# Optimization experiments

Hardware: AMD Instinct MI355X
Metric: run time of the kernel (lower is better)

The kernel has to match this reference:

```python
import jax, jax.numpy as jnp
import numpy as np

N, E = 30000, 240000          # nodes, edges per view
IN, D, OUT = 512, 128, 64      # in_dim, hidden_dim, out_dim
V, BLK, H, DM = 2, 2, 2, 64    # num_view, blk_size, num_heads, gate max-pool dim
NEG_ATT, NEG_OUT = 0.2, 0.01   # leaky_relu slopes (attention / outer)


def setup_inputs() -> dict:
    key = jax.random.key(0)
    ks = jax.random.split(key, 12)
    s = 0.05
    f32 = jnp.float32
    return {
        "ft": jax.random.normal(ks[0], (N, IN), f32),
        "src": jax.random.randint(ks[1], (V, E), 0, N, jnp.int32),
        "dst": jax.random.randint(ks[2], (V, E), 0, N, jnp.int32),
        "W_proj": jax.random.normal(ks[3], (IN, D), f32) * s,
        "W_embed": jax.random.normal(ks[4], (D, D), f32) * s,
        "a_l": jax.random.normal(ks[5], (V, BLK, H, D), f32) * s,
        "a_r": jax.random.normal(ks[6], (V, BLK, H, D), f32) * s,
        "Wv": jax.random.normal(ks[7], (V, BLK, H, D, D), f32) * s,
        "Wgm": jax.random.normal(ks[8], (V, BLK, D, DM), f32) * s,
        "Wgate": jax.random.normal(ks[9], (V, BLK, 2 * D + DM, H), f32) * s,
        "b_gate": jnp.zeros((V, BLK, H), f32),
        "W_tran": jax.random.normal(ks[10], (2 * D + DM and (D + V * H * D), OUT), f32) * s if False else jax.random.normal(ks[10], (D + V * H * D, OUT), f32) * s,
        "b_tran": jnp.zeros((OUT,), f32),
    }


def _seg_sum(x, idx):
    return jax.ops.segment_sum(x, idx, num_segments=N)


def _cgaan_layer(v, z, s_idx, d_idx, al, ar, wv, wgm, wgate, bg, merge):
    # v: [N,D] values, z: [N,D] attention features ('proj_z')
    # Multi-head attention logits: e_ij = leaky_relu(a_l.z_src + a_r.z_dst)  [E,H]
    logit_l = jnp.einsum("nd,hd->nh", z, al)
    logit_r = jnp.einsum("nd,hd->nh", z, ar)
    e = jax.nn.leaky_relu(logit_l[s_idx] + logit_r[d_idx], NEG_ATT)
    # edge softmax over incoming edges of each dst node
    m = jax.ops.segment_max(e, d_idx, num_segments=N)          # [N,H]
    ex = jnp.exp(e - m[d_idx])
    denom = _seg_sum(ex, d_idx)                                 # [N,H]
    alpha = ex / denom[d_idx]                                   # [E,H]
    # per-head value projection and weighted aggregation
    wvn = jnp.einsum("nd,hde->nhe", v, wv)                      # [N,H,D]
    agg = _seg_sum(alpha[:, :, None] * wvn[s_idx], d_idx)       # [N,H,D]
    # GaAN-style gate: sigmoid(FC([x_i, mean_j v_j, max_j (v_j Wgm)])) -> per-head scalar
    deg = _seg_sum(jnp.ones((s_idx.shape[0],), v.dtype), d_idx)  # [N]
    mean_n = _seg_sum(v[s_idx], d_idx) / jnp.maximum(deg, 1.0)[:, None]
    mx = jax.ops.segment_max((v @ wgm)[s_idx], d_idx, num_segments=N)
    mx = jnp.where(deg[:, None] > 0, mx, 0.0)                   # isolated nodes -> 0
    g = jax.nn.sigmoid(jnp.concatenate([v, mean_n, mx], -1) @ wgate + bg)  # [N,H]
    agg = g[:, :, None] * agg
    if merge == "mean":
        return agg.mean(axis=1)                                 # [N,D]
    return agg.reshape(agg.shape[0], -1)                        # cat -> [N,H*D]


def reference(ft, src, dst, W_proj, W_embed, a_l, a_r, Wv, Wgm, Wgate, b_gate, W_tran, b_tran):
    proj = ft @ W_proj                                          # [N,D]
    cur = [proj for _ in range(V)]
    for i in range(BLK):
        merge = "mean" if i < BLK - 1 else "cat"
        nxt = []
        for j in range(V):
            z = cur[j] @ W_embed
            h = _cgaan_layer(cur[j], z, src[j], dst[j], a_l[j, i], a_r[j, i],
                             Wv[j, i], Wgm[j, i], Wgate[j, i], b_gate[j, i], merge)
            nxt.append(jax.nn.leaky_relu(h, NEG_OUT))
        cur = nxt
    h = jnp.concatenate([proj] + cur, axis=-1)                  # [N, D+V*H*D]
    return h @ W_tran + b_tran
```

## Files before the change

### kernel.cpp

```cpp
#include <hip/hip_runtime.h>
#include <hip/hip_bf16.h>
#include <math.h>

#define NN 30000
#define EE 240000
#define IN_DIM 512
#define DD 128
#define OUTD 64
#define NV 2
#define NBLK 2
#define NH 2
#define DMM 64
#define NEG_ATT 0.2f
#define NEG_OUT 0.01f
#define CH 1024
#define NCH ((NN + CH - 1) / CH)

typedef __attribute__((ext_vector_type(8))) short bf16x8;
typedef __attribute__((ext_vector_type(4))) float f32x4;
typedef __attribute__((ext_vector_type(8))) unsigned short us8;

#define OFF_PROJVM 0
#define OFF_WV     131072
#define OFF_WGM    262144
#define OFF_TRAN   278528
#define WT_TOTAL   319488

__device__ __forceinline__ unsigned split_bf(float x) {
  unsigned u = __float_as_uint(x);
  unsigned hb = (u + 0x7FFFu + ((u >> 16) & 1u)) >> 16;
  float hf = __uint_as_float(hb << 16);
  float lo = x - hf;
  unsigned ul = __float_as_uint(lo);
  unsigned lb = (ul + 0x7FFFu + ((ul >> 16) & 1u)) >> 16;
  return hb | (lb << 16);
}

__device__ __forceinline__ void gload16(void* lds, const void* g) {
  __builtin_amdgcn_global_load_lds((const __attribute__((address_space(1))) unsigned int*)g,
                                   (__attribute__((address_space(3))) unsigned int*)lds, 16, 0, 0);
}

__global__ __launch_bounds__(256) void k_deg(const int* __restrict__ dst, int* __restrict__ deg) {
  int e = blockIdx.x * 256 + threadIdx.x;
  if (e < NV * EE) atomicAdd(&deg[(e / EE) * NN + dst[e]], 1);
}

__global__ __launch_bounds__(256) void k_scan1(const int* __restrict__ deg, int* __restrict__ partial) {
  int b = blockIdx.x, view = b / NCH, ch = b % NCH;
  const int* d = deg + view * NN + ch * CH;
  int rem = min(CH, NN - ch * CH);
  int t = threadIdx.x;
  int s = 0;
  for (int i = t; i < rem; i += 256) s += d[i];
  for (int k = 32; k; k >>= 1) s += __shfl_xor(s, k);
  __shared__ int wsum[4];
  if ((t & 63) == 0) wsum[t >> 6] = s;
  __syncthreads();
  if (t == 0) partial[b] = wsum[0] + wsum[1] + wsum[2] + wsum[3];
}

__global__ void k_scan2(const int* __restrict__ partial, int* __restrict__ chunkoff, int* __restrict__ off) {
  if (threadIdx.x == 0 && blockIdx.x == 0) {
    for (int v = 0; v < NV; v++) {
      int acc = 0;
      for (int c = 0; c < NCH; c++) { chunkoff[v * NCH + c] = acc; acc += partial[v * NCH + c]; }
      off[v * (NN + 1) + NN] = acc;
    }
  }
}

__global__ __launch_bounds__(256) void k_scan3(const int* __restrict__ deg, const int* __restrict__ chunkoff,
                                               int* __restrict__ off) {
  int b = blockIdx.x, view = b / NCH, ch = b % NCH;
  int base = ch * CH;
  const int* d = deg + view * NN;
  int* o = off + view * (NN + 1);
  int t = threadIdx.x, lane = t & 63, w = t >> 6;
  int i0 = base + t * 4;
  int x0 = 0, x1 = 0, x2 = 0, x3 = 0;
  if (i0 + 3 < NN) { int4 q = *(const int4*)(d + i0); x0 = q.x; x1 = q.y; x2 = q.z; x3 = q.w; }
  else {
    if (i0     < NN) x0 = d[i0];
    if (i0 + 1 < NN) x1 = d[i0 + 1];
    if (i0 + 2 < NN) x2 = d[i0 + 2];
  }
  int tot = x0 + x1 + x2 + x3;
  int incl = tot;
  for (int k = 1; k < 64; k <<= 1) { int y = __shfl_up(incl, k); if (lane >= k) incl += y; }
  __shared__ int wt[4];
  if (lane == 63) wt[w] = incl;
  __syncthreads();
  int wexcl = 0;
  for (int k = 0; k < w; k++) wexcl += wt[k];
  int excl = chunkoff[b] + wexcl + incl - tot;
  if (i0     < NN) o[i0]     = excl;
  if (i0 + 1 < NN) o[i0 + 1] = excl + x0;
  if (i0 + 2 < NN) o[i0 + 2] = excl + x0 + x1;
  if (i0 + 3 < NN) o[i0 + 3] = excl + x0 + x1 + x2;
}

__global__ __launch_bounds__(256) void k_fill(const int* __restrict__ src, const int* __restrict__ dst,
                                              const int* __restrict__ off, int* __restrict__ cursor,
                                              int* __restrict__ csr_src) {
  int e = blockIdx.x * 256 + threadIdx.x;
  if (e >= NV * EE) return;
  int view = e / EE;
  int d = dst[e];
  int p = atomicAdd(&cursor[view * NN + d], 1);
  csr_src[view * EE + off[view * (NN + 1) + d] + p] = src[e];
}

__global__ __launch_bounds__(256) void k_prep(const float* __restrict__ W_embed, const float* __restrict__ a_l,
                                              const float* __restrict__ a_r, float* __restrict__ Bl,
                                              float* __restrict__ Br) {
  int idx = blockIdx.x * 256 + threadIdx.x;
  if (idx >= NV * NBLK * DD * NH) return;
  int h = idx & 1, dd = (idx >> 1) & 127, lv = idx >> 8;
  const float* w = W_embed + dd * DD;
  const float* al = a_l + (lv * NH + h) * DD;
  const float* ar = a_r + (lv * NH + h) * DD;
  float sl = 0.f, sr = 0.f;
  for (int e = 0; e < DD; e++) { float we = w[e]; sl += we * al[e]; sr += we * ar[e]; }
  Bl[idx] = sl; Br[idx] = sr;
}

__global__ __launch_bounds__(256) void k_prep2(const float* __restrict__ Wp, const float* __restrict__ Wgm,
                                               float* __restrict__ wf) {
  int idx = blockIdx.x * 256 + threadIdx.x;
  int j = idx >> 15, k = (idx >> 6) & 511, n = idx & 63;
  const float* wp = Wp + (size_t)k * DD;
  const float* wg = Wgm + (size_t)(j * NBLK + 0) * DD * DMM + n;
  float s = 0.f;
  for (int e = 0; e < DD; e++) s += wp[e] * wg[(size_t)e * DMM];
  wf[idx] = s;
}

__global__ __launch_bounds__(256) void k_wsplit(const float* __restrict__ Wp, const float* __restrict__ wf,
                                                const float* __restrict__ Wv, const float* __restrict__ Wgm,
                                                const float* __restrict__ Wt,
                                                unsigned short* __restrict__ hi, unsigned short* __restrict__ lo) {
  int y = blockIdx.y;
  const float* src; int K, N; size_t doff;
  if (y == 0)      { src = Wp;                      K = 512; N = 128; doff = OFF_PROJVM; }
  else if (y <= 2) { int j = y - 1; src = wf + (size_t)j * 512 * 64; K = 512; N = 64; doff = OFF_PROJVM + (size_t)(128 + j * 64) * 512; }
  else if (y <= 6) { int lv = y - 3; src = Wv + (size_t)lv * 32768;  K = 256; N = 128; doff = OFF_WV + (size_t)lv * 32768; }
  else if (y <= 8) { int j = y - 7; src = Wgm + (size_t)(j * NBLK + 1) * 8192; K = 128; N = 64; doff = OFF_WGM + (size_t)j * 8192; }
  else             { src = Wt;                      K = 640; N = 64;  doff = OFF_TRAN; }
  int idx = blockIdx.x * 256 + threadIdx.x;
  if (idx >= K * N) return;
  int n = idx / K, k = idx % K;
  int tk = k >> 6, g = (k >> 3) & 7, j2 = k & 7;
  int ks = (tk << 6) | ((g ^ (n & 7)) << 3) | j2;
  unsigned p = split_bf(src[(size_t)k * N + n]);
  hi[doff + (size_t)n * K + ks] = (unsigned short)(p & 0xFFFFu);
  lo[doff + (size_t)n * K + ks] = (unsigned short)(p >> 16);
}

__global__ __launch_bounds__(256) void k_llr(const float* __restrict__ v0, const float* __restrict__ v1,
                                             int vstride,
                                             const float* __restrict__ Bl0, const float* __restrict__ Br0,
                                             const float* __restrict__ Bl1, const float* __restrict__ Br1,
                                             float* __restrict__ ll, float* __restrict__ lr) {
  int lane = threadIdx.x & 63, wid = threadIdx.x >> 6;
  int n = blockIdx.x * 4 + wid;
  int k = lane * 2;
  float2 a = *(const float2*)(v0 + (size_t)n * vstride + k);
  float2 b = *(const float2*)(v1 + (size_t)n * vstride + k);
  float r[8];
  r[0] = a.x * Bl0[k * 2]     + a.y * Bl0[k * 2 + 2];
  r[1] = a.x * Bl0[k * 2 + 1] + a.y * Bl0[k * 2 + 3];
  r[2] = a.x * Br0[k * 2]     + a.y * Br0[k * 2 + 2];
  r[3] = a.x * Br0[k * 2 + 1] + a.y * Br0[k * 2 + 3];
  r[4] = b.x * Bl1[k * 2]     + b.y * Bl1[k * 2 + 2];
  r[5] = b.x * Bl1[k * 2 + 1] + b.y * Bl1[k * 2 + 3];
  r[6] = b.x * Br1[k * 2]     + b.y * Br1[k * 2 + 2];
  r[7] = b.x * Br1[k * 2 + 1] + b.y * Br1[k * 2 + 3];
  for (int s = 32; s; s >>= 1)
#pragma unroll
    for (int q = 0; q < 8; q++) r[q] += __shfl_xor(r[q], s);
  if (lane == 0) {
    ll[n * 2] = r[0]; ll[n * 2 + 1] = r[1];
    lr[n * 2] = r[2]; lr[n * 2 + 1] = r[3];
    ll[NN * 2 + n * 2] = r[4]; ll[NN * 2 + n * 2 + 1] = r[5];
    lr[NN * 2 + n * 2] = r[6]; lr[NN * 2 + n * 2 + 1] = r[7];
  }
}

__global__ __launch_bounds__(256) void k_edge(const int* __restrict__ off_, const int* __restrict__ csr_,
                                              const float* __restrict__ ll_, const float* __restrict__ lr_,
                                              const float* __restrict__ v0, const float* __restrict__ v1,
                                              int vstride,
                                              const float* __restrict__ vmin,
                                              const float* __restrict__ Wg_, const float* __restrict__ bg_,
                                              float* __restrict__ S_) {
  int view = blockIdx.y;
  const int* off = off_ + view * (NN + 1);
  const int* csr = csr_ + (size_t)view * EE;
  const float* ll = ll_ + (size_t)view * NN * 2;
  const float* lr = lr_ + (size_t)view * NN * 2;
  const float* v = view ? v1 : v0;
  const float* vmi = vmin + view * 64;
  const float* Wg = Wg_ + (size_t)view * NBLK * (2 * DD + DMM) * NH;
  const float* bg = bg_ + view * NBLK * NH;
  float* S = S_ + (size_t)view * NN * (NH * DD);

  int lane = threadIdx.x & 63, wid = threadIdx.x >> 6;
  int n = blockIdx.x * 4 + wid;
  int e0 = off[n], nb = off[n + 1] - e0;
  size_t nS = (size_t)n * (NH * DD);
  int half = lane >> 5, hl = lane & 31;
  if (nb == 0) {
    *(float4*)(S + nS + half * DD + 4 * hl) = make_float4(0.f, 0.f, 0.f, 0.f);
    return;
  }
  float lr0 = lr[n * 2], lr1 = lr[n * 2 + 1];
  float sa0[4] = {0.f, 0.f, 0.f, 0.f}, sa1[4] = {0.f, 0.f, 0.f, 0.f}, vs[4] = {0.f, 0.f, 0.f, 0.f};
  float d0 = 0.f, d1 = 0.f, vm0 = -INFINITY, vm1 = -INFINITY;
  for (int base = 0; base < nb; base += 64) {
    int i = base + lane;
    float w0 = 0.f, w1 = 0.f, fv = 0.f; int sidx = 0;
    if (i < nb) {
      sidx = csr[e0 + i];
      float x0 = ll[sidx * 2] + lr0, x1 = ll[sidx * 2 + 1] + lr1;
      x0 = (x0 > 0.f) ? x0 : NEG_ATT * x0;
      x1 = (x1 > 0.f) ? x1 : NEG_ATT * x1;
      w0 = __expf(x0); w1 = __expf(x1); fv = 1.f;
    }
    d0 += w0; d1 += w1;
    int cnt = min(64, nb - base);
    for (int s = 0; 2 * s < cnt; s++) {
      int j = 2 * s + half;
      int se = __shfl(sidx, j);
      float we0 = __shfl(w0, j), we1 = __shfl(w1, j), fe = __shfl(fv, j);
      if (fe != 0.f) {
        float4 vv = *(const float4*)(v + (size_t)se * vstride + 4 * hl);
        sa0[0] += we0 * vv.x; sa0[1] += we0 * vv.y; sa0[2] += we0 * vv.z; sa0[3] += we0 * vv.w;
        sa1[0] += we1 * vv.x; sa1[1] += we1 * vv.y; sa1[2] += we1 * vv.z; sa1[3] += we1 * vv.w;
        vs[0] += vv.x; vs[1] += vv.y; vs[2] += vv.z; vs[3] += vv.w;
        float2 vm = *(const float2*)(vmi + (size_t)se * DD + 2 * hl);
        vm0 = fmaxf(vm0, vm.x); vm1 = fmaxf(vm1, vm.y);
      }
    }
  }
#pragma unroll
  for (int k = 0; k < 4; k++) {
    sa0[k] += __shfl_xor(sa0[k], 32);
    sa1[k] += __shfl_xor(sa1[k], 32);
    vs[k]  += __shfl_xor(vs[k], 32);
  }
  vm0 = fmaxf(vm0, __shfl_xor(vm0, 32));
  vm1 = fmaxf(vm1, __shfl_xor(vm1, 32));
  for (int s = 32; s; s >>= 1) { d0 += __shfl_xor(d0, s); d1 += __shfl_xor(d1, s); }
  float2 vn = *(const float2*)(v + (size_t)n * vstride + 2 * lane);
  float im = 1.f / (float)nb;
  float p0 = vn.x * Wg[(2 * lane) * 2]     + vn.y * Wg[(2 * lane + 1) * 2];
  float p1 = vn.x * Wg[(2 * lane) * 2 + 1] + vn.y * Wg[(2 * lane + 1) * 2 + 1];
  if (half == 0) {
#pragma unroll
    for (int k = 0; k < 4; k++) {
      float mk = vs[k] * im;
      p0 += mk * Wg[(128 + 4 * hl + k) * 2];
      p1 += mk * Wg[(128 + 4 * hl + k) * 2 + 1];
    }
  } else {
    p0 += vm0 * Wg[(256 + 2 * hl) * 2]     + vm1 * Wg[(256 + 2 * hl + 1) * 2];
    p1 += vm0 * Wg[(256 + 2 * hl) * 2 + 1] + vm1 * Wg[(256 + 2 * hl + 1) * 2 + 1];
  }
  for (int s = 32; s; s >>= 1) { p0 += __shfl_xor(p0, s); p1 += __shfl_xor(p1, s); }
  float g0 = 1.f / (1.f + __expf(-(p0 + bg[0])));
  float g1 = 1.f / (1.f + __expf(-(p1 + bg[1])));
  float q0 = g0 / d0, q1 = g1 / d1;
  float4 o4;
  if (half == 0) o4 = make_float4(sa0[0] * q0, sa0[1] * q0, sa0[2] * q0, sa0[3] * q0);
  else           o4 = make_float4(sa1[0] * q1, sa1[1] * q1, sa1[2] * q1, sa1[3] * q1);
  *(float4*)(S + nS + half * DD + 4 * hl) = o4;
}

struct GB {
  const float* A[4];
  unsigned long long bofs[4];
  float* C[4];
  int ldc[4];
};

template <int BN>
__global__ __launch_bounds__(256) void gemm_mfma(
    GB gb, const unsigned short* __restrict__ Bth, const unsigned short* __restrict__ Btl,
    int lda, int ldb, int M, int K,
    const float* __restrict__ bias, float fs, int flags) {
  constexpr int NSUB = BN / 32;
  constexpr int CPW = BN / 32;
  __shared__ __align__(16) unsigned short Ah[64][64], Al[64][64];
  __shared__ __align__(16) unsigned short Bh[BN][64], Bl[BN][64];
  const int z = blockIdx.z;
  const float* __restrict__ A = gb.A[z];
  float* __restrict__ C = gb.C[z];
  const int ldc = gb.ldc[z];
  const size_t bofs = gb.bofs[z];
  const int t = threadIdx.x;
  const int lane = t & 63, wv = t >> 6;
  const int lm = lane & 15, lg = lane >> 4;
  const int m0w = (wv & 1) * 32, n0w = (wv >> 1) * (BN / 2);
  const int row0 = blockIdx.x * 64;
  f32x4 acc[2][NSUB];
#pragma unroll
  for (int ms = 0; ms < 2; ms++)
#pragma unroll
    for (int ns = 0; ns < NSUB; ns++) acc[ms][ns] = (f32x4)0.f;

  float4 apre[2][2];
  const int ar_ = t >> 3, ag_ = t & 7;

  auto loadA = [&](int k0) {
#pragma unroll
    for (int q = 0; q < 2; q++) {
      int rr = row0 + q * 32 + ar_;
      if (rr < M) {
        const float* p = A + (size_t)rr * lda + k0 + ag_ * 8;
        apre[q][0] = *(const float4*)p;
        apre[q][1] = *(const float4*)(p + 4);
      } else {
        apre[q][0] = make_float4(0.f, 0.f, 0.f, 0.f);
        apre[q][1] = make_float4(0.f, 0.f, 0.f, 0.f);
      }
    }
  };
  auto storeA = [&]() {
#pragma unroll
    for (int q = 0; q < 2; q++) {
      int r = q * 32 + ar_;
      us8 h8, l8;
      float vals[8] = {apre[q][0].x, apre[q][0].y, apre[q][0].z, apre[q][0].w,
                       apre[q][1].x, apre[q][1].y, apre[q][1].z, apre[q][1].w};
#pragma unroll
      for (int e = 0; e < 8; e++) {
        unsigned pp = split_bf(vals[e]);
        h8[e] = (unsigned short)(pp & 0xFFFFu);
        l8[e] = (unsigned short)(pp >> 16);
      }
      int c = (ag_ ^ (r & 7)) << 3;
      *(us8*)&Ah[r][c] = h8;
      *(us8*)&Al[r][c] = l8;
    }
  };
  auto stageB = [&](int k0) {
#pragma unroll
    for (int q = 0; q < CPW; q++) {
      int chunk = wv * CPW + q;
      int o = chunk * 1024 + lane * 16;
      int n = o >> 7;
      int pq = (o >> 4) & 7;
      size_t gofs = bofs + (size_t)n * ldb + k0 + pq * 8;
      gload16((char*)&Bh[0][0] + o, Bth + gofs);
      gload16((char*)&Bl[0][0] + o, Btl + gofs);
    }
  };

  loadA(0);
  for (int k0 = 0; k0 < K; k0 += 64) {
    storeA();
    stageB(k0);
    __syncthreads();
    if (k0 + 64 < K) loadA(k0 + 64);
#pragma unroll
    for (int kc = 0; kc < 2; kc++) {
      bf16x8 afh[2], afl[2], bfh[NSUB], bfl[NSUB];
#pragma unroll
      for (int ms = 0; ms < 2; ms++) {
        int R = m0w + ms * 16 + lm;
        int c = (((kc * 4 + lg) ^ (R & 7)) << 3);
        afh[ms] = *(const bf16x8*)&Ah[R][c];
        afl[ms] = *(const bf16x8*)&Al[R][c];
      }
#pragma unroll
      for (int ns = 0; ns < NSUB; ns++) {
        int R = n0w + ns * 16 + lm;
        int c = (((kc * 4 + lg) ^ (R & 7)) << 3);
        bfh[ns] = *(const bf16x8*)&Bh[R][c];
        bfl[ns] = *(const bf16x8*)&Bl[R][c];
      }
#pragma unroll
      for (int ms = 0; ms < 2; ms++)
#pragma unroll
        for (int ns = 0; ns < NSUB; ns++) {
          acc[ms][ns] = __builtin_amdgcn_mfma_f32_16x16x32_bf16(afl[ms], bfh[ns], acc[ms][ns], 0, 0, 0);
          acc[ms][ns] = __builtin_amdgcn_mfma_f32_16x16x32_bf16(afh[ms], bfl[ns], acc[ms][ns], 0, 0, 0);
          acc[ms][ns] = __builtin_amdgcn_mfma_f32_16x16x32_bf16(afh[ms], bfh[ns], acc[ms][ns], 0, 0, 0);
        }
    }
    __syncthreads();
  }
#pragma unroll
  for (int ms = 0; ms < 2; ms++)
#pragma unroll
    for (int ns = 0; ns < NSUB; ns++)
#pragma unroll
      for (int j = 0; j < 4; j++) {
        int row = row0 + m0w + ms * 16 + lg * 4 + j;
        if (row >= M) continue;
        int col = n0w + ns * 16 + lm;
        float val = acc[ms][ns][j] * fs;
        if (bias) val += bias[col];
        if (flags & 2) val = (val > 0.f) ? val : NEG_OUT * val;
        C[(size_t)row * ldc + col] = val;
      }
}

extern "C" void kernel_launch(void* const* d_in, const int* in_sizes, int n_in,
                              void* d_out, int out_size, void* d_ws, size_t ws_size,
                              hipStream_t stream) {
  const float* ft      = (const float*)d_in[0];
  const int*   src     = (const int*)  d_in[1];
  const int*   dst     = (const int*)  d_in[2];
  const float* W_proj  = (const float*)d_in[3];
  const float* W_embed = (const float*)d_in[4];
  const float* a_l     = (const float*)d_in[5];
  const float* a_r     = (const float*)d_in[6];
  const float* Wv      = (const float*)d_in[7];
  const float* Wgm     = (const float*)d_in[8];
  const float* Wgate   = (const float*)d_in[9];
  const float* b_gate  = (const float*)d_in[10];
  const float* W_tran  = (const float*)d_in[11];
  const float* b_tran  = (const float*)d_in[12];
  float* out = (float*)d_out;
  char* ws = (char*)d_ws;
  (void)in_sizes; (void)n_in; (void)out_size; (void)ws_size;

  size_t o = 0;
  auto take = [&](size_t bytes) { size_t r = o; o += (bytes + 255) & ~(size_t)255; return r; };
  int*   deg     = (int*)(ws + take((size_t)NV * NN * 4));
  int*   cursor  = (int*)(ws + take((size_t)NV * NN * 4));
  int*   csr_off = (int*)(ws + take((size_t)NV * (NN + 1) * 4));
  int*   csr_src = (int*)(ws + take((size_t)NV * EE * 4));
  int*   partial = (int*)(ws + take((size_t)NV * NCH * 4));
  int*   chunkoff= (int*)(ws + take((size_t)NV * NCH * 4));
  float* Bl      = (float*)(ws + take((size_t)NV * NBLK * DD * NH * 4));
  float* Br      = (float*)(ws + take((size_t)NV * NBLK * DD * NH * 4));
  float* wf      = (float*)(ws + take((size_t)NV * 512 * 64 * 4));
  unsigned short* whi = (unsigned short*)(ws + take((size_t)WT_TOTAL * 2));
  unsigned short* wlo = (unsigned short*)(ws + take((size_t)WT_TOTAL * 2));
  float* h       = (float*)(ws + take((size_t)NN * 640 * 4));
  float* l0      = (float*)(ws + take((size_t)NV * NN * DD * 4));
  float* llb     = (float*)(ws + take((size_t)NV * NN * NH * 4));
  float* lrb     = (float*)(ws + take((size_t)NV * NN * NH * 4));
  float* vmb     = (float*)(ws + take((size_t)NN * 2 * DMM * 4));
  float* Sb      = (float*)(ws + take((size_t)NV * NN * NH * DD * 4));

  const int HSTR = 640;

  hipMemsetAsync(deg, 0, (size_t)(((size_t)NV * NN * 4 + 255) & ~(size_t)255) + (size_t)NV * NN * 4, stream);
  k_deg<<<(NV * EE + 255) / 256, 256, 0, stream>>>(dst, deg);
  k_scan1<<<NV * NCH, 256, 0, stream>>>(deg, partial);
  k_scan2<<<1, 64, 0, stream>>>(partial, chunkoff, csr_off);
  k_scan3<<<NV * NCH, 256, 0, stream>>>(deg, chunkoff, csr_off);
  k_fill<<<(NV * EE + 255) / 256, 256, 0, stream>>>(src, dst, csr_off, cursor, csr_src);
  k_prep<<<(NV * NBLK * DD * NH + 255) / 256, 256, 0, stream>>>(W_embed, a_l, a_r, Bl, Br);
  k_prep2<<<256, 256, 0, stream>>>(W_proj, Wgm, wf);
  k_wsplit<<<dim3(256, 10), 256, 0, stream>>>(W_proj, wf, Wv, Wgm, W_tran, whi, wlo);

  const int GM = (NN + 63) / 64;

  {
    GB gb = {{ft, ft, ft, ft},
             {OFF_PROJVM, OFF_PROJVM + (size_t)128 * 512, 0, 0},
             {h, vmb, nullptr, nullptr},
             {HSTR, 128, 0, 0}};
    gemm_mfma<128><<<dim3(GM, 1, 2), 256, 0, stream>>>(gb, whi, wlo, IN_DIM, 512, NN, 512,
                                                       nullptr, 1.f, 0);
  }

  for (int i = 0; i < NBLK; i++) {
    const float* v0 = (i == 0) ? h : l0;
    const float* v1 = (i == 0) ? h : l0 + (size_t)NN * DD;
    int vst = (i == 0) ? HSTR : DD;
    if (i == 1) {
      GB gb = {{l0, l0 + (size_t)NN * DD, nullptr, nullptr},
               {OFF_WGM, OFF_WGM + 8192, 0, 0},
               {vmb, vmb + 64, nullptr, nullptr},
               {128, 128, 0, 0}};
      gemm_mfma<64><<<dim3(GM, 1, 2), 256, 0, stream>>>(gb, whi, wlo, DD, 128, NN, 128,
                                                        nullptr, 1.f, 0);
    }
    k_llr<<<NN / 4, 256, 0, stream>>>(v0, v1, vst,
                                      Bl + (0 * NBLK + i) * 256, Br + (0 * NBLK + i) * 256,
                                      Bl + (1 * NBLK + i) * 256, Br + (1 * NBLK + i) * 256,
                                      llb, lrb);
    k_edge<<<dim3(NN / 4, 2), 256, 0, stream>>>(csr_off, csr_src, llb, lrb, v0, v1, vst, vmb,
                                                Wgate + (size_t)i * (2 * DD + DMM) * NH,
                                                b_gate + i * NH, Sb);
    if (i == 0) {
      GB gb = {{Sb, Sb + (size_t)NN * 256, nullptr, nullptr},
               {OFF_WV, OFF_WV + 2 * 32768, 0, 0},
               {l0, l0 + (size_t)NN * DD, nullptr, nullptr},
               {DD, DD, 0, 0}};
      gemm_mfma<128><<<dim3(GM, 1, 2), 256, 0, stream>>>(gb, whi, wlo, 256, 256, NN, 256,
                                                         nullptr, 0.5f, 2);
    } else {
      GB gb = {{Sb, Sb + 128, Sb + (size_t)NN * 256, Sb + (size_t)NN * 256 + 128},
               {OFF_WV + 1 * 32768, OFF_WV + 1 * 32768 + 128,
                OFF_WV + 3 * 32768, OFF_WV + 3 * 32768 + 128},
               {h + 128, h + 256, h + 384, h + 512},
               {HSTR, HSTR, HSTR, HSTR}};
      gemm_mfma<128><<<dim3(GM, 1, 4), 256, 0, stream>>>(gb, whi, wlo, 256, 256, NN, 128,
                                                         nullptr, 1.f, 2);
    }
  }
  {
    GB gb = {{h, nullptr, nullptr, nullptr}, {OFF_TRAN, 0, 0, 0}, {out, nullptr, nullptr, nullptr},
             {OUTD, 0, 0, 0}};
    gemm_mfma<64><<<dim3(GM, 1, 1), 256, 0, stream>>>(gb, whi, wlo, HSTR, 640, NN, 640,
                                                      b_tran, 1.f, 0);
  }
}
```

Baseline: 369.4 us.

## Store intermediate activations as packed bf16 and load GEMM A tiles directly to LDS

Intermediate node features, gate max-pool inputs and aggregated edge outputs are now written as packed bf16 rows (value plus vm columns together) instead of fp32. The gather-heavy edge kernel then reads half the bytes per neighbor. The GEMMs that consume these buffers skip the hi/lo split of A, using global_load_lds and one fewer MFMA per tile. This gives up accuracy on the activations, since they lose their low bf16 part, and the buffer layout is restructured across stages.

After: 328.6 us. -11.1%, faster.

```diff
diff --git a/kernel.cpp b/kernel.cpp
--- a/kernel.cpp
+++ b/kernel.cpp
@@ -18,6 +18,7 @@
 
 typedef __attribute__((ext_vector_type(8))) short bf16x8;
 typedef __attribute__((ext_vector_type(4))) float f32x4;
+typedef __attribute__((ext_vector_type(4))) unsigned short us4;
 typedef __attribute__((ext_vector_type(8))) unsigned short us8;
 
 #define OFF_PROJVM 0
@@ -34,6 +35,14 @@
   unsigned ul = __float_as_uint(lo);
   unsigned lb = (ul + 0x7FFFu + ((ul >> 16) & 1u)) >> 16;
   return hb | (lb << 16);
+}
+
+__device__ __forceinline__ unsigned short f2bf(float x) {
+  unsigned u = __float_as_uint(x);
+  return (unsigned short)((u + 0x7FFFu + ((u >> 16) & 1u)) >> 16);
+}
+__device__ __forceinline__ float bf2f(unsigned short u) {
+  return __uint_as_float((unsigned)u << 16);
 }
 
 __device__ __forceinline__ void gload16(void* lds, const void* g) {
@@ -157,25 +166,27 @@
   lo[doff + (size_t)n * K + ks] = (unsigned short)(p >> 16);
 }
 
-__global__ __launch_bounds__(256) void k_llr(const float* __restrict__ v0, const float* __restrict__ v1,
-                                             int vstride,
+__global__ __launch_bounds__(256) void k_llr(const unsigned short* __restrict__ p0,
+                                             const unsigned short* __restrict__ p1, int ps,
                                              const float* __restrict__ Bl0, const float* __restrict__ Br0,
                                              const float* __restrict__ Bl1, const float* __restrict__ Br1,
                                              float* __restrict__ ll, float* __restrict__ lr) {
   int lane = threadIdx.x & 63, wid = threadIdx.x >> 6;
   int n = blockIdx.x * 4 + wid;
   int k = lane * 2;
-  float2 a = *(const float2*)(v0 + (size_t)n * vstride + k);
-  float2 b = *(const float2*)(v1 + (size_t)n * vstride + k);
+  unsigned a = *(const unsigned*)(p0 + (size_t)n * ps + k);
+  unsigned b = *(const unsigned*)(p1 + (size_t)n * ps + k);
+  float ax = bf2f((unsigned short)a), ay = bf2f((unsigned short)(a >> 16));
+  float bx = bf2f((unsigned short)b), by = bf2f((unsigned short)(b >> 16));
   float r[8];
-  r[0] = a.x * Bl0[k * 2]     + a.y * Bl0[k * 2 + 2];
-  r[1] = a.x * Bl0[k * 2 + 1] + a.y * Bl0[k * 2 + 3];
-  r[2] = a.x * Br0[k * 2]     + a.y * Br0[k * 2 + 2];
-  r[3] = a.x * Br0[k * 2 + 1] + a.y * Br0[k * 2 + 3];
-  r[4] = b.x * Bl1[k * 2]     + b.y * Bl1[k * 2 + 2];
-  r[5] = b.x * Bl1[k * 2 + 1] + b.y * Bl1[k * 2 + 3];
-  r[6] = b.x * Br1[k * 2]     + b.y * Br1[k * 2 + 2];
-  r[7] = b.x * Br1[k * 2 + 1] + b.y * Br1[k * 2 + 3];
+  r[0] = ax * Bl0[k * 2]     + ay * Bl0[k * 2 + 2];
+  r[1] = ax * Bl0[k * 2 + 1] + ay * Bl0[k * 2 + 3];
+  r[2] = ax * Br0[k * 2]     + ay * Br0[k * 2 + 2];
+  r[3] = ax * Br0[k * 2 + 1] + ay * Br0[k * 2 + 3];
+  r[4] = bx * Bl1[k * 2]     + by * Bl1[k * 2 + 2];
+  r[5] = bx * Bl1[k * 2 + 1] + by * Bl1[k * 2 + 3];
+  r[6] = bx * Br1[k * 2]     + by * Br1[k * 2 + 2];
+  r[7] = bx * Br1[k * 2 + 1] + by * Br1[k * 2 + 3];
   for (int s = 32; s; s >>= 1)
 #pragma unroll
     for (int q = 0; q < 8; q++) r[q] += __shfl_xor(r[q], s);
@@ -189,29 +200,28 @@
 
 __global__ __launch_bounds__(256) void k_edge(const int* __restrict__ off_, const int* __restrict__ csr_,
                                               const float* __restrict__ ll_, const float* __restrict__ lr_,
-                                              const float* __restrict__ v0, const float* __restrict__ v1,
-                                              int vstride,
-                                              const float* __restrict__ vmin,
+                                              const unsigned short* __restrict__ pk_, long viewStride,
+                                              int ps, int vmoff0, int vmstep,
                                               const float* __restrict__ Wg_, const float* __restrict__ bg_,
-                                              float* __restrict__ S_) {
+                                              unsigned short* __restrict__ S_) {
   int view = blockIdx.y;
   const int* off = off_ + view * (NN + 1);
   const int* csr = csr_ + (size_t)view * EE;
   const float* ll = ll_ + (size_t)view * NN * 2;
   const float* lr = lr_ + (size_t)view * NN * 2;
-  const float* v = view ? v1 : v0;
-  const float* vmi = vmin + view * 64;
+  const unsigned short* pk = pk_ + (size_t)view * viewStride;
+  int vmoff = vmoff0 + view * vmstep;
   const float* Wg = Wg_ + (size_t)view * NBLK * (2 * DD + DMM) * NH;
   const float* bg = bg_ + view * NBLK * NH;
-  float* S = S_ + (size_t)view * NN * (NH * DD);
+  unsigned short* S = S_ + (size_t)view * NN * 256;
 
   int lane = threadIdx.x & 63, wid = threadIdx.x >> 6;
   int n = blockIdx.x * 4 + wid;
   int e0 = off[n], nb = off[n + 1] - e0;
-  size_t nS = (size_t)n * (NH * DD);
   int half = lane >> 5, hl = lane & 31;
   if (nb == 0) {
-    *(float4*)(S + nS + half * DD + 4 * hl) = make_float4(0.f, 0.f, 0.f, 0.f);
+    us4 z4 = {0, 0, 0, 0};
+    *(us4*)(S + (size_t)n * 256 + half * 128 + 4 * hl) = z4;
     return;
   }
   float lr0 = lr[n * 2], lr1 = lr[n * 2 + 1];
@@ -234,12 +244,15 @@
       int se = __shfl(sidx, j);
       float we0 = __shfl(w0, j), we1 = __shfl(w1, j), fe = __shfl(fv, j);
       if (fe != 0.f) {
-        float4 vv = *(const float4*)(v + (size_t)se * vstride + 4 * hl);
-        sa0[0] += we0 * vv.x; sa0[1] += we0 * vv.y; sa0[2] += we0 * vv.z; sa0[3] += we0 * vv.w;
-        sa1[0] += we1 * vv.x; sa1[1] += we1 * vv.y; sa1[2] += we1 * vv.z; sa1[3] += we1 * vv.w;
-        vs[0] += vv.x; vs[1] += vv.y; vs[2] += vv.z; vs[3] += vv.w;
-        float2 vm = *(const float2*)(vmi + (size_t)se * DD + 2 * hl);
-        vm0 = fmaxf(vm0, vm.x); vm1 = fmaxf(vm1, vm.y);
+        const unsigned short* rowp = pk + (size_t)se * ps;
+        us4 vq = *(const us4*)(rowp + 4 * hl);
+        float v0 = bf2f(vq[0]), v1 = bf2f(vq[1]), v2 = bf2f(vq[2]), v3 = bf2f(vq[3]);
+        sa0[0] += we0 * v0; sa0[1] += we0 * v1; sa0[2] += we0 * v2; sa0[3] += we0 * v3;
+        sa1[0] += we1 * v0; sa1[1] += we1 * v1; sa1[2] += we1 * v2; sa1[3] += we1 * v3;
+        vs[0] += v0; vs[1] += v1; vs[2] += v2; vs[3] += v3;
+        unsigned vmu = *(const unsigned*)(rowp + vmoff + 2 * hl);
+        vm0 = fmaxf(vm0, bf2f((unsigned short)vmu));
+        vm1 = fmaxf(vm1, bf2f((unsigned short)(vmu >> 16)));
       }
     }
   }
@@ -252,10 +265,11 @@
   vm0 = fmaxf(vm0, __shfl_xor(vm0, 32));
   vm1 = fmaxf(vm1, __shfl_xor(vm1, 32));
   for (int s = 32; s; s >>= 1) { d0 += __shfl_xor(d0, s); d1 += __shfl_xor(d1, s); }
-  float2 vn = *(const float2*)(v + (size_t)n * vstride + 2 * lane);
+  unsigned vnu = *(const unsigned*)(pk + (size_t)n * ps + 2 * lane);
+  float vnx = bf2f((unsigned short)vnu), vny = bf2f((unsigned short)(vnu >> 16));
   float im = 1.f / (float)nb;
-  float p0 = vn.x * Wg[(2 * lane) * 2]     + vn.y * Wg[(2 * lane + 1) * 2];
-  float p1 = vn.x * Wg[(2 * lane) * 2 + 1] + vn.y * Wg[(2 * lane + 1) * 2 + 1];
+  float p0 = vnx * Wg[(2 * lane) * 2]     + vny * Wg[(2 * lane + 1) * 2];
+  float p1 = vnx * Wg[(2 * lane) * 2 + 1] + vny * Wg[(2 * lane + 1) * 2 + 1];
   if (half == 0) {
 #pragma unroll
     for (int k = 0; k < 4; k++) {
@@ -271,32 +285,42 @@
   float g0 = 1.f / (1.f + __expf(-(p0 + bg[0])));
   float g1 = 1.f / (1.f + __expf(-(p1 + bg[1])));
   float q0 = g0 / d0, q1 = g1 / d1;
-  float4 o4;
-  if (half == 0) o4 = make_float4(sa0[0] * q0, sa0[1] * q0, sa0[2] * q0, sa0[3] * q0);
-  else           o4 = make_float4(sa1[0] * q1, sa1[1] * q1, sa1[2] * q1, sa1[3] * q1);
-  *(float4*)(S + nS + half * DD + 4 * hl) = o4;
+  us4 o4;
+  if (half == 0) {
+    o4[0] = f2bf(sa0[0] * q0); o4[1] = f2bf(sa0[1] * q0);
+    o4[2] = f2bf(sa0[2] * q0); o4[3] = f2bf(sa0[3] * q0);
+  } else {
+    o4[0] = f2bf(sa1[0] * q1); o4[1] = f2bf(sa1[1] * q1);
+    o4[2] = f2bf(sa1[2] * q1); o4[3] = f2bf(sa1[3] * q1);
+  }
+  *(us4*)(S + (size_t)n * 256 + half * 128 + 4 * hl) = o4;
 }
 
 struct GB {
-  const float* A[4];
+  const void* A[4];
   unsigned long long bofs[4];
   float* C[4];
+  unsigned short* P[4];
   int ldc[4];
+  int pldc[4];
 };
 
-template <int BN>
+template <int BN, bool ABF>
 __global__ __launch_bounds__(256) void gemm_mfma(
     GB gb, const unsigned short* __restrict__ Bth, const unsigned short* __restrict__ Btl,
     int lda, int ldb, int M, int K,
     const float* __restrict__ bias, float fs, int flags) {
   constexpr int NSUB = BN / 32;
   constexpr int CPW = BN / 32;
-  __shared__ __align__(16) unsigned short Ah[64][64], Al[64][64];
+  __shared__ __align__(16) unsigned short Ah[64][64];
+  __shared__ __align__(16) unsigned short Al[ABF ? 2 : 64][64];
   __shared__ __align__(16) unsigned short Bh[BN][64], Bl[BN][64];
   const int z = blockIdx.z;
-  const float* __restrict__ A = gb.A[z];
+  const float* __restrict__ Af = (const float*)gb.A[z];
+  const unsigned short* __restrict__ Ab = (const unsigned short*)gb.A[z];
   float* __restrict__ C = gb.C[z];
-  const int ldc = gb.ldc[z];
+  unsigned short* __restrict__ P = gb.P[z];
+  const int ldc = gb.ldc[z], pldc = gb.pldc[z];
   const size_t bofs = gb.bofs[z];
   const int t = threadIdx.x;
   const int lane = t & 63, wv = t >> 6;
@@ -313,35 +337,51 @@
   const int ar_ = t >> 3, ag_ = t & 7;
 
   auto loadA = [&](int k0) {
-#pragma unroll
-    for (int q = 0; q < 2; q++) {
-      int rr = row0 + q * 32 + ar_;
-      if (rr < M) {
-        const float* p = A + (size_t)rr * lda + k0 + ag_ * 8;
-        apre[q][0] = *(const float4*)p;
-        apre[q][1] = *(const float4*)(p + 4);
-      } else {
-        apre[q][0] = make_float4(0.f, 0.f, 0.f, 0.f);
-        apre[q][1] = make_float4(0.f, 0.f, 0.f, 0.f);
+    if constexpr (!ABF) {
+#pragma unroll
+      for (int q = 0; q < 2; q++) {
+        int rr = row0 + q * 32 + ar_;
+        if (rr < M) {
+          const float* p = Af + (size_t)rr * lda + k0 + ag_ * 8;
+          apre[q][0] = *(const float4*)p;
+          apre[q][1] = *(const float4*)(p + 4);
+        } else {
+          apre[q][0] = make_float4(0.f, 0.f, 0.f, 0.f);
+          apre[q][1] = make_float4(0.f, 0.f, 0.f, 0.f);
+        }
       }
     }
   };
   auto storeA = [&]() {
-#pragma unroll
-    for (int q = 0; q < 2; q++) {
-      int r = q * 32 + ar_;
-      us8 h8, l8;
-      float vals[8] = {apre[q][0].x, apre[q][0].y, apre[q][0].z, apre[q][0].w,
-                       apre[q][1].x, apre[q][1].y, apre[q][1].z, apre[q][1].w};
-#pragma unroll
-      for (int e = 0; e < 8; e++) {
-        unsigned pp = split_bf(vals[e]);
-        h8[e] = (unsigned short)(pp & 0xFFFFu);
-        l8[e] = (unsigned short)(pp >> 16);
-      }
-      int c = (ag_ ^ (r & 7)) << 3;
-      *(us8*)&Ah[r][c] = h8;
-      *(us8*)&Al[r][c] = l8;
+    if constexpr (!ABF) {
+#pragma unroll
+      for (int q = 0; q < 2; q++) {
+        int r = q * 32 + ar_;
+        us8 h8, l8;
+        float vals[8] = {apre[q][0].x, apre[q][0].y, apre[q][0].z, apre[q][0].w,
+                         apre[q][1].x, apre[q][1].y, apre[q][1].z, apre[q][1].w};
+#pragma unroll
+        for (int e = 0; e < 8; e++) {
+          unsigned pp = split_bf(vals[e]);
+          h8[e] = (unsigned short)(pp & 0xFFFFu);
+          l8[e] = (unsigned short)(pp >> 16);
+        }
+        int c = (ag_ ^ (r & 7)) << 3;
+        *(us8*)&Ah[r][c] = h8;
+        *(us8*)&Al[r][c] = l8;
+      }
+    }
+  };
+  auto stageA_bf = [&](int k0) {
+    if constexpr (ABF) {
+#pragma unroll
+      for (int q = 0; q < 2; q++) {
+        int r = q * 32 + ar_;
+        int rr = min(row0 + r, M - 1);
+        int scg = ag_ ^ (r & 7);
+        gload16((char*)&Ah[0][0] + q * 4096 + t * 16,
+                Ab + (size_t)rr * lda + k0 + scg * 8);
+      }
     }
   };
   auto stageB = [&](int k0) {
@@ -359,10 +399,10 @@
 
   loadA(0);
   for (int k0 = 0; k0 < K; k0 += 64) {
-    storeA();
+    if constexpr (ABF) stageA_bf(k0); else storeA();
     stageB(k0);
     __syncthreads();
-    if (k0 + 64 < K) loadA(k0 + 64);
+    if constexpr (!ABF) { if (k0 + 64 < K) loadA(k0 + 64); }
 #pragma unroll
     for (int kc = 0; kc < 2; kc++) {
       bf16x8 afh[2], afl[2], bfh[NSUB], bfl[NSUB];
@@ -371,7 +411,7 @@
         int R = m0w + ms * 16 + lm;
         int c = (((kc * 4 + lg) ^ (R & 7)) << 3);
         afh[ms] = *(const bf16x8*)&Ah[R][c];
-        afl[ms] = *(const bf16x8*)&Al[R][c];
+        if constexpr (!ABF) afl[ms] = *(const bf16x8*)&Al[R][c];
       }
 #pragma unroll
       for (int ns = 0; ns < NSUB; ns++) {
@@ -384,7 +424,8 @@
       for (int ms = 0; ms < 2; ms++)
 #pragma unroll
         for (int ns = 0; ns < NSUB; ns++) {
-          acc[ms][ns] = __builtin_amdgcn_mfma_f32_16x16x32_bf16(afl[ms], bfh[ns], acc[ms][ns], 0, 0, 0);
+          if constexpr (!ABF)
+            acc[ms][ns] = __builtin_amdgcn_mfma_f32_16x16x32_bf16(afl[ms], bfh[ns], acc[ms][ns], 0, 0, 0);
           acc[ms][ns] = __builtin_amdgcn_mfma_f32_16x16x32_bf16(afh[ms], bfl[ns], acc[ms][ns], 0, 0, 0);
           acc[ms][ns] = __builtin_amdgcn_mfma_f32_16x16x32_bf16(afh[ms], bfh[ns], acc[ms][ns], 0, 0, 0);
         }
@@ -403,7 +444,8 @@
         float val = acc[ms][ns][j] * fs;
         if (bias) val += bias[col];
         if (flags & 2) val = (val > 0.f) ? val : NEG_OUT * val;
-        C[(size_t)row * ldc + col] = val;
+        if (C) C[(size_t)row * ldc + col] = val;
+        if (P) P[(size_t)row * pldc + col] = f2bf(val);
       }
 }
 
@@ -441,11 +483,11 @@
   unsigned short* whi = (unsigned short*)(ws + take((size_t)WT_TOTAL * 2));
   unsigned short* wlo = (unsigned short*)(ws + take((size_t)WT_TOTAL * 2));
   float* h       = (float*)(ws + take((size_t)NN * 640 * 4));
-  float* l0      = (float*)(ws + take((size_t)NV * NN * DD * 4));
+  unsigned short* pk0 = (unsigned short*)(ws + take((size_t)NN * 256 * 2));
+  unsigned short* pk1 = (unsigned short*)(ws + take((size_t)NV * NN * 192 * 2));
+  unsigned short* Sbf = (unsigned short*)(ws + take((size_t)NV * NN * 256 * 2));
   float* llb     = (float*)(ws + take((size_t)NV * NN * NH * 4));
   float* lrb     = (float*)(ws + take((size_t)NV * NN * NH * 4));
-  float* vmb     = (float*)(ws + take((size_t)NN * 2 * DMM * 4));
-  float* Sb      = (float*)(ws + take((size_t)NV * NN * NH * DD * 4));
 
   const int HSTR = 640;
 
@@ -462,54 +504,64 @@
   const int GM = (NN + 63) / 64;
 
   {
-    GB gb = {{ft, ft, ft, ft},
-             {OFF_PROJVM, OFF_PROJVM + (size_t)128 * 512, 0, 0},
-             {h, vmb, nullptr, nullptr},
-             {HSTR, 128, 0, 0}};
-    gemm_mfma<128><<<dim3(GM, 1, 2), 256, 0, stream>>>(gb, whi, wlo, IN_DIM, 512, NN, 512,
-                                                       nullptr, 1.f, 0);
-  }
-
-  for (int i = 0; i < NBLK; i++) {
-    const float* v0 = (i == 0) ? h : l0;
-    const float* v1 = (i == 0) ? h : l0 + (size_t)NN * DD;
-    int vst = (i == 0) ? HSTR : DD;
-    if (i == 1) {
-      GB gb = {{l0, l0 + (size_t)NN * DD, nullptr, nullptr},
-               {OFF_WGM, OFF_WGM + 8192, 0, 0},
-               {vmb, vmb + 64, nullptr, nullptr},
-               {128, 128, 0, 0}};
-      gemm_mfma<64><<<dim3(GM, 1, 2), 256, 0, stream>>>(gb, whi, wlo, DD, 128, NN, 128,
-                                                        nullptr, 1.f, 0);
-    }
-    k_llr<<<NN / 4, 256, 0, stream>>>(v0, v1, vst,
-                                      Bl + (0 * NBLK + i) * 256, Br + (0 * NBLK + i) * 256,
-                                      Bl + (1 * NBLK + i) * 256, Br + (1 * NBLK + i) * 256,
-                                      llb, lrb);
-    k_edge<<<dim3(NN / 4, 2), 256, 0, stream>>>(csr_off, csr_src, llb, lrb, v0, v1, vst, vmb,
-                                                Wgate + (size_t)i * (2 * DD + DMM) * NH,
-                                                b_gate + i * NH, Sb);
-    if (i == 0) {
-      GB gb = {{Sb, Sb + (size_t)NN * 256, nullptr, nullptr},
-               {OFF_WV, OFF_WV + 2 * 32768, 0, 0},
-               {l0, l0 + (size_t)NN * DD, nullptr, nullptr},
-               {DD, DD, 0, 0}};
-      gemm_mfma<128><<<dim3(GM, 1, 2), 256, 0, stream>>>(gb, whi, wlo, 256, 256, NN, 256,
-                                                         nullptr, 0.5f, 2);
-    } else {
-      GB gb = {{Sb, Sb + 128, Sb + (size_t)NN * 256, Sb + (size_t)NN * 256 + 128},
-               {OFF_WV + 1 * 32768, OFF_WV + 1 * 32768 + 128,
-                OFF_WV + 3 * 32768, OFF_WV + 3 * 32768 + 128},
-               {h + 128, h + 256, h + 384, h + 512},
-               {HSTR, HSTR, HSTR, HSTR}};
-      gemm_mfma<128><<<dim3(GM, 1, 4), 256, 0, stream>>>(gb, whi, wlo, 256, 256, NN, 128,
-                                                         nullptr, 1.f, 2);
-    }
-  }
+    GB gb = {};
+    gb.A[0] = ft; gb.A[1] = ft;
+    gb.bofs[0] = OFF_PROJVM; gb.bofs[1] = OFF_PROJVM + (size_t)128 * 512;
+    gb.C[0] = h;  gb.ldc[0] = HSTR;
+    gb.P[0] = pk0;       gb.pldc[0] = 256;
+    gb.P[1] = pk0 + 128; gb.pldc[1] = 256;
+    gemm_mfma<128, false><<<dim3(GM, 1, 2), 256, 0, stream>>>(gb, whi, wlo, IN_DIM, 512, NN, 512,
+                                                              nullptr, 1.f, 0);
+  }
+
+  k_llr<<<NN / 4, 256, 0, stream>>>(pk0, pk0, 256,
+                                    Bl + 0 * 256, Br + 0 * 256, Bl + 2 * 256, Br + 2 * 256, llb, lrb);
+  k_edge<<<dim3(NN / 4, 2), 256, 0, stream>>>(csr_off, csr_src, llb, lrb,
+                                              pk0, 0L, 256, 128, 64,
+                                              Wgate, b_gate, Sbf);
   {
-    GB gb = {{h, nullptr, nullptr, nullptr}, {OFF_TRAN, 0, 0, 0}, {out, nullptr, nullptr, nullptr},
-             {OUTD, 0, 0, 0}};
-    gemm_mfma<64><<<dim3(GM, 1, 1), 256, 0, stream>>>(gb, whi, wlo, HSTR, 640, NN, 640,
-                                                      b_tran, 1.f, 0);
-  }
-}
+    GB gb = {};
+    for (int j = 0; j < 2; j++) {
+      gb.A[j] = Sbf + (size_t)j * NN * 256;
+      gb.bofs[j] = OFF_WV + (size_t)(j * 2) * 32768;
+      gb.P[j] = pk1 + (size_t)j * NN * 192;
+      gb.pldc[j] = 192;
+    }
+    gemm_mfma<128, true><<<dim3(GM, 1, 2), 256, 0, stream>>>(gb, whi, wlo, 256, 256, NN, 256,
+                                                             nullptr, 0.5f, 2);
+  }
+  {
+    GB gb = {};
+    for (int j = 0; j < 2; j++) {
+      gb.A[j] = pk1 + (size_t)j * NN * 192;
+      gb.bofs[j] = OFF_WGM + (size_t)j * 8192;
+      gb.P[j] = pk1 + (size_t)j * NN * 192 + 128;
+      gb.pldc[j] = 192;
+    }
+    gemm_mfma<64, true><<<dim3(GM, 1, 2), 256, 0, stream>>>(gb, whi, wlo, 192, 128, NN, 128,
+                                                            nullptr, 1.f, 0);
+  }
+  k_llr<<<NN / 4, 256, 0, stream>>>(pk1, pk1 + (size_t)NN * 192, 192,
+                                    Bl + 1 * 256, Br + 1 * 256, Bl + 3 * 256, Br + 3 * 256, llb, lrb);
+  k_edge<<<dim3(NN / 4, 2), 256, 0, stream>>>(csr_off, csr_src, llb, lrb,
+                                              pk1, (long)NN * 192, 192, 128, 0,
+                                              Wgate + (size_t)(2 * DD + DMM) * NH, b_gate + NH, Sbf);
+  {
+    GB gb = {};
+    for (int z = 0; z < 4; z++) {
+      int j = z >> 1, hd = z & 1;
+      gb.A[z] = Sbf + (size_t)j * NN * 256 + hd * 128;
+      gb.bofs[z] = OFF_WV + (size_t)(j * 2 + 1) * 32768 + hd * 128;
+      gb.C[z] = h + 128 + z * 128;
+      gb.ldc[z] = HSTR;
+    }
+    gemm_mfma<128, true><<<dim3(GM, 1, 4), 256, 0, stream>>>(gb, whi, wlo, 256, 256, NN, 128,
+                                                             nullptr, 1.f, 2);
+  }
+  {
+    GB gb = {};
+    gb.A[0] = h; gb.bofs[0] = OFF_TRAN; gb.C[0] = out; gb.ldc[0] = OUTD;
+    gemm_mfma<64, false><<<dim3(GM, 1, 1), 256, 0, stream>>>(gb, whi, wlo, HSTR, 640, NN, 640,
+                                                             b_tran, 1.f, 0);
+  }
+}
```
